# Performance work log

Hardware: AMD Instinct MI355X
Metric: run time of the kernel (lower is better)

Reference implementation:

```python
import jax, jax.numpy as jnp
import numpy as np

NUM_GRAPHS = 8
EV_A3_TO_GPA = 160.21766208


def _energy(pos, bond_vec, src, dst, edge_graph, centers, W1, b1, W2, b2, W3, b3):
    # Surrogate GNN energy: edge displacement mixes pos and bond_vec so both get grads,
    # mirroring grad(total_energies, [pos, bond_vec]) in the original wrapper.
    disp = bond_vec + pos[dst] - pos[src]                      # [E,3]
    d = jnp.sqrt(jnp.sum(disp * disp, axis=-1) + 1e-12)        # [E]
    rbf = jnp.exp(-jnp.square(d[:, None] - centers[None, :]))  # [E,K]
    h = jax.nn.silu(rbf @ W1 + b1)                             # [E,H]
    h = jax.nn.silu(h @ W2 + b2)                               # [E,H]
    e_edge = (h @ W3 + b3)[:, 0]                               # [E]
    return jax.ops.segment_sum(e_edge, edge_graph, num_segments=NUM_GRAPHS)  # [B]


def setup_inputs() -> dict:
    key = jax.random.key(0)
    ks = jax.random.split(key, 8)
    N, E, K, H = 49152, 786432, 32, 64
    pos = jax.random.normal(ks[0], (N, 3), jnp.float32) * 3.0
    bond_vec = jax.random.normal(ks[1], (E, 3), jnp.float32)
    src = jax.random.randint(ks[2], (E,), 0, N, dtype=jnp.int32)
    dst = jax.random.randint(ks[3], (E,), 0, N, dtype=jnp.int32)
    edge_graph = jnp.repeat(jnp.arange(NUM_GRAPHS, dtype=jnp.int32), E // NUM_GRAPHS)
    volume = jax.random.uniform(ks[4], (N,), jnp.float32, 50.0, 150.0)
    centers = jnp.linspace(0.0, 5.0, K).astype(jnp.float32)
    W1 = jax.random.normal(ks[5], (K, H), jnp.float32) / np.float32(np.sqrt(K))
    b1 = jnp.zeros((H,), jnp.float32)
    W2 = jax.random.normal(ks[6], (H, H), jnp.float32) / np.float32(np.sqrt(H))
    b2 = jnp.zeros((H,), jnp.float32)
    W3 = jax.random.normal(ks[7], (H, 1), jnp.float32) / np.float32(np.sqrt(H))
    b3 = jnp.zeros((1,), jnp.float32)
    return {"pos": pos, "bond_vec": bond_vec, "src": src, "dst": dst,
            "edge_graph": edge_graph, "volume": volume, "centers": centers,
            "W1": W1, "b1": b1, "W2": W2, "b2": b2, "W3": W3, "b3": b3}


def reference(pos, bond_vec, src, dst, edge_graph, volume, centers, W1, b1, W2, b2, W3, b3):
    energies, vjp_fn = jax.vjp(
        lambda p, bv: _energy(p, bv, src, dst, edge_graph, centers, W1, b1, W2, b2, W3, b3),
        pos, bond_vec)
    # grad_outputs = ones_like(total_energies)
    gpos, gbv = vjp_fn(jnp.ones_like(energies))
    forces = -gpos                                             # [N,3]
    f_ij = -gbv                                                # [E,3]
    # Per-graph stress: bond_vec_g^T @ f_ij_g, vectorized as segment-summed outer products.
    outer = bond_vec[:, :, None] * f_ij[:, None, :]            # [E,3,3]
    S = jax.ops.segment_sum(outer, edge_graph, num_segments=NUM_GRAPHS)  # [B,3,3]
    nodes_per_graph = pos.shape[0] // NUM_GRAPHS
    vol0 = volume[jnp.arange(NUM_GRAPHS) * nodes_per_graph]    # volume at first node of each graph
    stresses = (-EV_A3_TO_GPA * S / vol0[:, None, None]).reshape(NUM_GRAPHS * 3, 3)
    hessian = jnp.zeros((1,), jnp.float32)                     # calc_hessian=False
    return energies, forces, stresses, hessian
```

## Files before the change

kernel.cpp:

```cpp
#include <hip/hip_runtime.h>
#include <math.h>

#define K_RBF 32
#define H_DIM 64
#define TBL 4096
#define D_MAX 16.0f
#define N_NODES 49152
#define N_EDGES 786432
#define N_GRAPHS 8
#define NODES_PER_GRAPH 6144
#define EV_A3_TO_GPA 160.21766208f
#define LOG2E 1.44269504088896f

#define OUT_FORCES 8
#define OUT_STRESS 147464
#define OUT_TAIL_N 81

#define CHUNK_NODES  192
#define CHUNK_FLOATS 576
#define N_CHUNKS     256
#define REC_CAP      7168

#define EDGE_BLOCKS   384
#define EDGE_THREADS  1024
#define EDGES_PER_GRAPH (N_EDGES / N_GRAPHS)
#define BLK_PER_GRAPH 48

#define OFF_TAB 0u
#define OFF_CNT 32768u
#define OFF_REC 33792u
#define WS_NEED (OFF_REC + (size_t)N_CHUNKS * REC_CAP * 16u)

__device__ __forceinline__ int chunk_of(int node) {
    return (int)((unsigned)((node >> 6) * 683) >> 11);
}

__global__ __launch_bounds__(256) void build_table(
    const float* __restrict__ centers,
    const float* __restrict__ W1, const float* __restrict__ b1,
    const float* __restrict__ W2, const float* __restrict__ b2,
    const float* __restrict__ W3, const float* __restrict__ b3,
    float2* __restrict__ tab, int* __restrict__ gcnt,
    float* __restrict__ out, int zero_out_tail)
{
    if (blockIdx.x == 0) {
        int t = threadIdx.x;
        gcnt[t] = 0;
        if (zero_out_tail) {
            if (t < N_GRAPHS) out[t] = 0.f;
            else if (t < OUT_TAIL_N) out[3 * N_NODES + t] = 0.f;
        }
    }

    __shared__ float W2s[H_DIM * 65];
    for (int idx = threadIdx.x; idx < H_DIM * H_DIM; idx += 256)
        W2s[(idx >> 6) * 65 + (idx & 63)] = W2[idx];
    __syncthreads();

    int lane = threadIdx.x & 63;
    int i    = blockIdx.x * 4 + (threadIdx.x >> 6);
    float d  = (float)i * (D_MAX / (float)TBL);

    float z1 = b1[lane], u = 0.f;
#pragma unroll
    for (int k = 0; k < K_RBF; ++k) {
        float tc = d - centers[k];
        float e  = exp2f(-tc * tc * LOG2E);
        float w  = W1[k * H_DIM + lane];
        z1 = fmaf(e, w, z1);
        u  = fmaf(-2.f * tc * e, w, u);
    }
    float s1  = 1.f / (1.f + exp2f(-z1 * LOG2E));
    float h1  = z1 * s1;
    float ds1 = s1 * fmaf(z1, 1.f - s1, 1.f);

    float z2 = b2[lane];
#pragma unroll
    for (int h = 0; h < H_DIM; ++h)
        z2 = fmaf(__shfl(h1, h, 64), W2s[h * 65 + lane], z2);

    float s2  = 1.f / (1.f + exp2f(-z2 * LOG2E));
    float w3  = W3[lane];
    float Fp  = z2 * s2 * w3;
    float dz2 = w3 * s2 * fmaf(z2, 1.f - s2, 1.f);

    float dh1 = 0.f;
#pragma unroll
    for (int j = 0; j < H_DIM; ++j)
        dh1 = fmaf(__shfl(dz2, j, 64), W2s[lane * 65 + j], dh1);

    float Gp = dh1 * ds1 * u;
#pragma unroll
    for (int m = 32; m > 0; m >>= 1) {
        Fp += __shfl_xor(Fp, m, 64);
        Gp += __shfl_xor(Gp, m, 64);
    }
    if (lane == 0) tab[i] = make_float2(Fp + b3[0], Gp);
}

__global__ __launch_bounds__(EDGE_THREADS) void edge_compute(
    const float* __restrict__ pos, const float* __restrict__ bond,
    const int* __restrict__ src, const int* __restrict__ dst,
    const float* __restrict__ volume, const float2* __restrict__ tab,
    float4* __restrict__ recs, int* __restrict__ gcnt,
    float* __restrict__ out)
{
    __shared__ int   cnt[N_CHUNKS];
    __shared__ int   basech[N_CHUNKS];
    __shared__ float red[16][10];

    const int t = threadIdx.x;
    if (t < N_CHUNKS) cnt[t] = 0;
    __syncthreads();

    const int g = blockIdx.x & 7;
    const int w = blockIdx.x >> 3;
    const int base_e = g * EDGES_PER_GRAPH + w * (EDGE_THREADS * 2);

    float vacc[10];
#pragma unroll
    for (int q = 0; q < 10; ++q) vacc[q] = 0.f;

    int   edi[2], esi[2], es0[2], es1[2];
    float egx[2], egy[2], egz[2];

#pragma unroll
    for (int i = 0; i < 2; ++i) {
        int e  = base_e + i * EDGE_THREADS + t;
        int si = src[e], di = dst[e];
        float bx = bond[3 * e + 0], by = bond[3 * e + 1], bz = bond[3 * e + 2];
        float dx = bx + pos[3 * di + 0] - pos[3 * si + 0];
        float dy = by + pos[3 * di + 1] - pos[3 * si + 1];
        float dz = bz + pos[3 * di + 2] - pos[3 * si + 2];
        float d  = sqrtf(fmaf(dx, dx, fmaf(dy, dy, fmaf(dz, dz, 1e-12f))));

        float tt  = fminf(d * ((float)TBL / D_MAX), (float)(TBL - 1));
        int   ix  = min((int)tt, TBL - 2);
        float fr  = tt - (float)ix;
        float2 ta = tab[ix], tb2 = tab[ix + 1];
        float F = fmaf(fr, tb2.x - ta.x, ta.x);
        float G = fmaf(fr, tb2.y - ta.y, ta.y);

        float scl = G / d;
        float gx = scl * dx, gy = scl * dy, gz = scl * dz;
        egx[i] = gx; egy[i] = gy; egz[i] = gz;
        edi[i] = di; esi[i] = si;
        es0[i] = atomicAdd(&cnt[chunk_of(di)], 1);
        es1[i] = atomicAdd(&cnt[chunk_of(si)], 1);

        vacc[0] += F;
        vacc[1] = fmaf(bx, gx, vacc[1]); vacc[2] = fmaf(bx, gy, vacc[2]);
        vacc[3] = fmaf(bx, gz, vacc[3]); vacc[4] = fmaf(by, gx, vacc[4]);
        vacc[5] = fmaf(by, gy, vacc[5]); vacc[6] = fmaf(by, gz, vacc[6]);
        vacc[7] = fmaf(bz, gx, vacc[7]); vacc[8] = fmaf(bz, gy, vacc[8]);
        vacc[9] = fmaf(bz, gz, vacc[9]);
    }
    __syncthreads();
    if (t < N_CHUNKS) basech[t] = atomicAdd(&gcnt[t], cnt[t]);
    __syncthreads();
#pragma unroll
    for (int i = 0; i < 2; ++i) {
        int c0 = chunk_of(edi[i]), c1 = chunk_of(esi[i]);
        int l0 = edi[i] - c0 * CHUNK_NODES;
        int l1 = esi[i] - c1 * CHUNK_NODES;
        int p0 = basech[c0] + es0[i];
        int p1 = basech[c1] + es1[i];
        if (p0 < REC_CAP)
            recs[(size_t)c0 * REC_CAP + p0] =
                make_float4(-egx[i], -egy[i], -egz[i], __int_as_float(l0));
        if (p1 < REC_CAP)
            recs[(size_t)c1 * REC_CAP + p1] =
                make_float4(egx[i], egy[i], egz[i], __int_as_float(l1));
    }

#pragma unroll
    for (int q = 0; q < 10; ++q) {
        float x = vacc[q];
#pragma unroll
        for (int m = 32; m > 0; m >>= 1) x += __shfl_xor(x, m, 64);
        vacc[q] = x;
    }
    int wave = t >> 6;
    if ((t & 63) == 0)
#pragma unroll
        for (int q = 0; q < 10; ++q) red[wave][q] = vacc[q];
    __syncthreads();
    if (t < 10) {
        float tot = 0.f;
#pragma unroll
        for (int k = 0; k < 16; ++k) tot += red[k][t];
        if (t == 0) atomicAdd(out + g, tot);
        else {
            float vol = volume[g * NODES_PER_GRAPH];
            atomicAdd(out + OUT_STRESS + g * 9 + (t - 1),
                      tot * (EV_A3_TO_GPA / vol));
        }
    }
}

__global__ __launch_bounds__(512) void scatter_direct(
    const float4* __restrict__ recs, const int* __restrict__ gcnt,
    float* __restrict__ out)
{
    __shared__ float acc[CHUNK_FLOATS];
    const int t = threadIdx.x;
    if (t < CHUNK_FLOATS) acc[t] = 0.f;
    if (t < CHUNK_FLOATS - 512) acc[512 + t] = 0.f;
    __syncthreads();

    const int c = blockIdx.x;
    int total = min(gcnt[c], REC_CAP);
    const float4* seg = recs + (size_t)c * REC_CAP;
    for (int r = t; r < total; r += 512) {
        float4 rec = seg[r];
        int li = 3 * __float_as_int(rec.w);
        atomicAdd(&acc[li + 0], rec.x);
        atomicAdd(&acc[li + 1], rec.y);
        atomicAdd(&acc[li + 2], rec.z);
    }
    __syncthreads();

    if (t < CHUNK_FLOATS / 4) {
        float4* dst4 = (float4*)(out + OUT_FORCES + c * CHUNK_FLOATS);
        dst4[t] = ((const float4*)acc)[t];
    }
}

__global__ __launch_bounds__(256) void edge_fallback(
    const float* __restrict__ pos, const float* __restrict__ bond,
    const int* __restrict__ src, const int* __restrict__ dst,
    const float* __restrict__ volume, const float2* __restrict__ tab,
    float* __restrict__ out)
{
    __shared__ float red[4][10];
    int lb = (blockIdx.x & 7) * (EDGES_PER_GRAPH / 256) + (blockIdx.x >> 3);
    int g  = blockIdx.x & 7;
    int e  = lb * 256 + threadIdx.x;

    int si = src[e], di = dst[e];
    float bx = bond[3 * e + 0], by = bond[3 * e + 1], bz = bond[3 * e + 2];
    float dx = bx + pos[3 * di + 0] - pos[3 * si + 0];
    float dy = by + pos[3 * di + 1] - pos[3 * si + 1];
    float dz = bz + pos[3 * di + 2] - pos[3 * si + 2];
    float d  = sqrtf(fmaf(dx, dx, fmaf(dy, dy, fmaf(dz, dz, 1e-12f))));

    float tt  = fminf(d * ((float)TBL / D_MAX), (float)(TBL - 1));
    int   ix  = min((int)tt, TBL - 2);
    float fr  = tt - (float)ix;
    float2 ta = tab[ix], tb2 = tab[ix + 1];
    float F = fmaf(fr, tb2.x - ta.x, ta.x);
    float G = fmaf(fr, tb2.y - ta.y, ta.y);
    float scl = G / d;
    float gx = scl * dx, gy = scl * dy, gz = scl * dz;

    float* forces = out + OUT_FORCES;
    atomicAdd(forces + 3 * di + 0, -gx);
    atomicAdd(forces + 3 * di + 1, -gy);
    atomicAdd(forces + 3 * di + 2, -gz);
    atomicAdd(forces + 3 * si + 0,  gx);
    atomicAdd(forces + 3 * si + 1,  gy);
    atomicAdd(forces + 3 * si + 2,  gz);

    float v[10] = { F,
                    bx * gx, bx * gy, bx * gz,
                    by * gx, by * gy, by * gz,
                    bz * gx, bz * gy, bz * gz };
#pragma unroll
    for (int q = 0; q < 10; ++q) {
        float x = v[q];
#pragma unroll
        for (int m = 32; m > 0; m >>= 1) x += __shfl_xor(x, m, 64);
        v[q] = x;
    }
    int wave = threadIdx.x >> 6;
    if ((threadIdx.x & 63) == 0)
#pragma unroll
        for (int q = 0; q < 10; ++q) red[wave][q] = v[q];
    __syncthreads();
    if (threadIdx.x < 10) {
        float tot = red[0][threadIdx.x] + red[1][threadIdx.x]
                  + red[2][threadIdx.x] + red[3][threadIdx.x];
        if (threadIdx.x == 0) atomicAdd(out + g, tot);
        else {
            float vol = volume[g * NODES_PER_GRAPH];
            atomicAdd(out + OUT_STRESS + g * 9 + (threadIdx.x - 1),
                      tot * (EV_A3_TO_GPA / vol));
        }
    }
}

extern "C" void kernel_launch(void* const* d_in, const int* in_sizes, int n_in,
                              void* d_out, int out_size, void* d_ws, size_t ws_size,
                              hipStream_t stream)
{
    const float* pos     = (const float*)d_in[0];
    const float* bond    = (const float*)d_in[1];
    const int*   src     = (const int*)d_in[2];
    const int*   dst     = (const int*)d_in[3];
    const float* volume  = (const float*)d_in[5];
    const float* centers = (const float*)d_in[6];
    const float* W1 = (const float*)d_in[7];
    const float* b1 = (const float*)d_in[8];
    const float* W2 = (const float*)d_in[9];
    const float* b2 = (const float*)d_in[10];
    const float* W3 = (const float*)d_in[11];
    const float* b3 = (const float*)d_in[12];
    float*  out  = (float*)d_out;
    char*   ws   = (char*)d_ws;
    float2* tab  = (float2*)(ws + OFF_TAB);
    int*    gcnt = (int*)(ws + OFF_CNT);
    float4* recs = (float4*)(ws + OFF_REC);

    if (ws_size >= WS_NEED) {
        build_table<<<TBL / 4, 256, 0, stream>>>(centers, W1, b1, W2, b2, W3, b3,
                                                 tab, gcnt, out, 1);
        edge_compute<<<EDGE_BLOCKS, EDGE_THREADS, 0, stream>>>(
            pos, bond, src, dst, volume, tab, recs, gcnt, out);
        scatter_direct<<<N_CHUNKS, 512, 0, stream>>>(recs, gcnt, out);
    } else {
        hipMemsetAsync(d_out, 0, (size_t)out_size * sizeof(float), stream);
        build_table<<<TBL / 4, 256, 0, stream>>>(centers, W1, b1, W2, b2, W3, b3,
                                                 tab, gcnt, out, 0);
        edge_fallback<<<N_EDGES / 256, 256, 0, stream>>>(
            pos, bond, src, dst, volume, tab, out);
    }
}
```

Baseline: 150.7 us.

## Replace chunked record binning with per-node slots and gather reduction

Drops the chunked binning, where each block counted edges per 192-node chunk in shared memory and then claimed space with per-chunk global atomics, in favour of fixed per-node slots of capacity 96. Each edge endpoint now takes its slot with a global atomicAdd on a per-node counter. A new gather kernel uses four threads per node to sum that node's records and writes the forces directly, with no shared-memory float atomics. The trade is two returning global atomics per edge at random addresses, scattered record writes, and a much larger workspace. If the workspace is too small the slow fallback path runs, and records past 96 for a node are silently dropped.

```diff
diff --git a/kernel.cpp b/kernel.cpp
--- a/kernel.cpp
+++ b/kernel.cpp
@@ -16,10 +16,7 @@
 #define OUT_STRESS 147464
 #define OUT_TAIL_N 81
 
-#define CHUNK_NODES  192
-#define CHUNK_FLOATS 576
-#define N_CHUNKS     256
-#define REC_CAP      7168
+#define CAP_DEG 96
 
 #define EDGE_BLOCKS   384
 #define EDGE_THREADS  1024
@@ -28,37 +25,33 @@
 
 #define OFF_TAB 0u
 #define OFF_CNT 32768u
-#define OFF_REC 33792u
-#define WS_NEED (OFF_REC + (size_t)N_CHUNKS * REC_CAP * 16u)
-
-__device__ __forceinline__ int chunk_of(int node) {
-    return (int)((unsigned)((node >> 6) * 683) >> 11);
-}
+#define OFF_REC 229376u
+#define WS_NEED (OFF_REC + (size_t)N_NODES * CAP_DEG * 16u)
 
 __global__ __launch_bounds__(256) void build_table(
     const float* __restrict__ centers,
     const float* __restrict__ W1, const float* __restrict__ b1,
     const float* __restrict__ W2, const float* __restrict__ b2,
     const float* __restrict__ W3, const float* __restrict__ b3,
-    float2* __restrict__ tab, int* __restrict__ gcnt,
-    float* __restrict__ out, int zero_out_tail)
-{
-    if (blockIdx.x == 0) {
-        int t = threadIdx.x;
-        gcnt[t] = 0;
-        if (zero_out_tail) {
+    float2* __restrict__ tab, int* __restrict__ ncnt,
+    float* __restrict__ out, int main_path)
+{
+    const int t = threadIdx.x;
+    if (main_path) {
+        if (t < 48) ncnt[blockIdx.x * 48 + t] = 0;
+        if (blockIdx.x == 0) {
             if (t < N_GRAPHS) out[t] = 0.f;
             else if (t < OUT_TAIL_N) out[3 * N_NODES + t] = 0.f;
         }
     }
 
     __shared__ float W2s[H_DIM * 65];
-    for (int idx = threadIdx.x; idx < H_DIM * H_DIM; idx += 256)
+    for (int idx = t; idx < H_DIM * H_DIM; idx += 256)
         W2s[(idx >> 6) * 65 + (idx & 63)] = W2[idx];
     __syncthreads();
 
-    int lane = threadIdx.x & 63;
-    int i    = blockIdx.x * 4 + (threadIdx.x >> 6);
+    int lane = t & 63;
+    int i    = blockIdx.x * 4 + (t >> 6);
     float d  = (float)i * (D_MAX / (float)TBL);
 
     float z1 = b1[lane], u = 0.f;
@@ -102,17 +95,12 @@
     const float* __restrict__ pos, const float* __restrict__ bond,
     const int* __restrict__ src, const int* __restrict__ dst,
     const float* __restrict__ volume, const float2* __restrict__ tab,
-    float4* __restrict__ recs, int* __restrict__ gcnt,
+    float4* __restrict__ recs, int* __restrict__ ncnt,
     float* __restrict__ out)
 {
-    __shared__ int   cnt[N_CHUNKS];
-    __shared__ int   basech[N_CHUNKS];
     __shared__ float red[16][10];
 
     const int t = threadIdx.x;
-    if (t < N_CHUNKS) cnt[t] = 0;
-    __syncthreads();
-
     const int g = blockIdx.x & 7;
     const int w = blockIdx.x >> 3;
     const int base_e = g * EDGES_PER_GRAPH + w * (EDGE_THREADS * 2);
@@ -121,7 +109,7 @@
 #pragma unroll
     for (int q = 0; q < 10; ++q) vacc[q] = 0.f;
 
-    int   edi[2], esi[2], es0[2], es1[2];
+    int   edi[2], esi[2], ep0[2], ep1[2];
     float egx[2], egy[2], egz[2];
 
 #pragma unroll
@@ -145,8 +133,8 @@
         float gx = scl * dx, gy = scl * dy, gz = scl * dz;
         egx[i] = gx; egy[i] = gy; egz[i] = gz;
         edi[i] = di; esi[i] = si;
-        es0[i] = atomicAdd(&cnt[chunk_of(di)], 1);
-        es1[i] = atomicAdd(&cnt[chunk_of(si)], 1);
+        ep0[i] = atomicAdd(&ncnt[di], 1);
+        ep1[i] = atomicAdd(&ncnt[si], 1);
 
         vacc[0] += F;
         vacc[1] = fmaf(bx, gx, vacc[1]); vacc[2] = fmaf(bx, gy, vacc[2]);
@@ -155,22 +143,15 @@
         vacc[7] = fmaf(bz, gx, vacc[7]); vacc[8] = fmaf(bz, gy, vacc[8]);
         vacc[9] = fmaf(bz, gz, vacc[9]);
     }
-    __syncthreads();
-    if (t < N_CHUNKS) basech[t] = atomicAdd(&gcnt[t], cnt[t]);
-    __syncthreads();
+
 #pragma unroll
     for (int i = 0; i < 2; ++i) {
-        int c0 = chunk_of(edi[i]), c1 = chunk_of(esi[i]);
-        int l0 = edi[i] - c0 * CHUNK_NODES;
-        int l1 = esi[i] - c1 * CHUNK_NODES;
-        int p0 = basech[c0] + es0[i];
-        int p1 = basech[c1] + es1[i];
-        if (p0 < REC_CAP)
-            recs[(size_t)c0 * REC_CAP + p0] =
-                make_float4(-egx[i], -egy[i], -egz[i], __int_as_float(l0));
-        if (p1 < REC_CAP)
-            recs[(size_t)c1 * REC_CAP + p1] =
-                make_float4(egx[i], egy[i], egz[i], __int_as_float(l1));
+        if (ep0[i] < CAP_DEG)
+            recs[(size_t)edi[i] * CAP_DEG + ep0[i]] =
+                make_float4(-egx[i], -egy[i], -egz[i], 0.f);
+        if (ep1[i] < CAP_DEG)
+            recs[(size_t)esi[i] * CAP_DEG + ep1[i]] =
+                make_float4(egx[i], egy[i], egz[i], 0.f);
     }
 
 #pragma unroll
@@ -198,31 +179,29 @@
     }
 }
 
-__global__ __launch_bounds__(512) void scatter_direct(
-    const float4* __restrict__ recs, const int* __restrict__ gcnt,
+__global__ __launch_bounds__(256) void gather_forces(
+    const float4* __restrict__ recs, const int* __restrict__ ncnt,
     float* __restrict__ out)
 {
-    __shared__ float acc[CHUNK_FLOATS];
-    const int t = threadIdx.x;
-    if (t < CHUNK_FLOATS) acc[t] = 0.f;
-    if (t < CHUNK_FLOATS - 512) acc[512 + t] = 0.f;
-    __syncthreads();
-
-    const int c = blockIdx.x;
-    int total = min(gcnt[c], REC_CAP);
-    const float4* seg = recs + (size_t)c * REC_CAP;
-    for (int r = t; r < total; r += 512) {
-        float4 rec = seg[r];
-        int li = 3 * __float_as_int(rec.w);
-        atomicAdd(&acc[li + 0], rec.x);
-        atomicAdd(&acc[li + 1], rec.y);
-        atomicAdd(&acc[li + 2], rec.z);
-    }
-    __syncthreads();
-
-    if (t < CHUNK_FLOATS / 4) {
-        float4* dst4 = (float4*)(out + OUT_FORCES + c * CHUNK_FLOATS);
-        dst4[t] = ((const float4*)acc)[t];
+    const int tid  = blockIdx.x * 256 + threadIdx.x;
+    const int node = tid >> 2;
+    const int sub  = tid & 3;
+    if (node >= N_NODES) return;
+
+    const int cnt = min(ncnt[node], CAP_DEG);
+    const float4* seg = recs + (size_t)node * CAP_DEG;
+
+    float sx = 0.f, sy = 0.f, sz = 0.f;
+    for (int k = sub; k < cnt; k += 4) {
+        float4 r = seg[k];
+        sx += r.x; sy += r.y; sz += r.z;
+    }
+    sx += __shfl_xor(sx, 1, 64); sy += __shfl_xor(sy, 1, 64); sz += __shfl_xor(sz, 1, 64);
+    sx += __shfl_xor(sx, 2, 64); sy += __shfl_xor(sy, 2, 64); sz += __shfl_xor(sz, 2, 64);
+
+    if (sub < 3) {
+        float v = (sub == 0) ? sx : ((sub == 1) ? sy : sz);
+        out[OUT_FORCES + node * 3 + sub] = v;
     }
 }
 
@@ -308,19 +287,19 @@
     float*  out  = (float*)d_out;
     char*   ws   = (char*)d_ws;
     float2* tab  = (float2*)(ws + OFF_TAB);
-    int*    gcnt = (int*)(ws + OFF_CNT);
+    int*    ncnt = (int*)(ws + OFF_CNT);
     float4* recs = (float4*)(ws + OFF_REC);
 
     if (ws_size >= WS_NEED) {
         build_table<<<TBL / 4, 256, 0, stream>>>(centers, W1, b1, W2, b2, W3, b3,
-                                                 tab, gcnt, out, 1);
+                                                 tab, ncnt, out, 1);
         edge_compute<<<EDGE_BLOCKS, EDGE_THREADS, 0, stream>>>(
-            pos, bond, src, dst, volume, tab, recs, gcnt, out);
-        scatter_direct<<<N_CHUNKS, 512, 0, stream>>>(recs, gcnt, out);
+            pos, bond, src, dst, volume, tab, recs, ncnt, out);
+        gather_forces<<<(N_NODES * 4) / 256, 256, 0, stream>>>(recs, ncnt, out);
     } else {
         hipMemsetAsync(d_out, 0, (size_t)out_size * sizeof(float), stream);
         build_table<<<TBL / 4, 256, 0, stream>>>(centers, W1, b1, W2, b2, W3, b3,
-                                                 tab, gcnt, out, 0);
+                                                 tab, ncnt, out, 0);
         edge_fallback<<<N_EDGES / 256, 256, 0, stream>>>(
             pos, bond, src, dst, volume, tab, out);
     }
```

After: 200.0 us. +32.8%, slower.

## Replace LDS float atomics in force scatter with counting-sort segmented reduction

Applied to the files above, without the earlier changes.

The per-chunk force scatter now counts records per node using integer LDS atomics, prefix-scans the counts, places records into a sorted LDS buffer, and has one thread per (node, component) sum its contiguous segment. This replaces three float atomicAdds per record with one integer atomic plus a serial per-thread sum, and gives a deterministic summation order. The edge kernel also changes from 384x1024 to 512x768 blocks. The sort uses about 112 KB of LDS per block, which limits occupancy, and the final sum loops are unbalanced across threads when node degrees differ.

```diff
diff --git a/kernel.cpp b/kernel.cpp
--- a/kernel.cpp
+++ b/kernel.cpp
@@ -17,14 +17,16 @@
 #define OUT_TAIL_N 81
 
 #define CHUNK_NODES  192
-#define CHUNK_FLOATS 576
 #define N_CHUNKS     256
 #define REC_CAP      7168
 
-#define EDGE_BLOCKS   384
-#define EDGE_THREADS  1024
+#define EDGE_BLOCKS   512
+#define EDGE_THREADS  768
 #define EDGES_PER_GRAPH (N_EDGES / N_GRAPHS)
-#define BLK_PER_GRAPH 48
+#define BLK_PER_GRAPH 64
+
+#define SCT_THREADS 576
+#define SCT_ITERS   13
 
 #define OFF_TAB 0u
 #define OFF_CNT 32768u
@@ -107,7 +109,7 @@
 {
     __shared__ int   cnt[N_CHUNKS];
     __shared__ int   basech[N_CHUNKS];
-    __shared__ float red[16][10];
+    __shared__ float red[12][10];
 
     const int t = threadIdx.x;
     if (t < N_CHUNKS) cnt[t] = 0;
@@ -188,7 +190,7 @@
     if (t < 10) {
         float tot = 0.f;
 #pragma unroll
-        for (int k = 0; k < 16; ++k) tot += red[k][t];
+        for (int k = 0; k < 12; ++k) tot += red[k][t];
         if (t == 0) atomicAdd(out + g, tot);
         else {
             float vol = volume[g * NODES_PER_GRAPH];
@@ -198,31 +200,68 @@
     }
 }
 
-__global__ __launch_bounds__(512) void scatter_direct(
+__global__ __launch_bounds__(SCT_THREADS) void scatter_sort(
     const float4* __restrict__ recs, const int* __restrict__ gcnt,
     float* __restrict__ out)
 {
-    __shared__ float acc[CHUNK_FLOATS];
+    __shared__ float4 sorted[REC_CAP];
+    __shared__ int    cnt[CHUNK_NODES];
+    __shared__ int    scan[CHUNK_NODES];
+
     const int t = threadIdx.x;
-    if (t < CHUNK_FLOATS) acc[t] = 0.f;
-    if (t < CHUNK_FLOATS - 512) acc[512 + t] = 0.f;
-    __syncthreads();
-
     const int c = blockIdx.x;
-    int total = min(gcnt[c], REC_CAP);
+    if (t < CHUNK_NODES) cnt[t] = 0;
+    __syncthreads();
+
+    const int total = min(gcnt[c], REC_CAP);
     const float4* seg = recs + (size_t)c * REC_CAP;
-    for (int r = t; r < total; r += 512) {
-        float4 rec = seg[r];
-        int li = 3 * __float_as_int(rec.w);
-        atomicAdd(&acc[li + 0], rec.x);
-        atomicAdd(&acc[li + 1], rec.y);
-        atomicAdd(&acc[li + 2], rec.z);
-    }
-    __syncthreads();
-
-    if (t < CHUNK_FLOATS / 4) {
-        float4* dst4 = (float4*)(out + OUT_FORCES + c * CHUNK_FLOATS);
-        dst4[t] = ((const float4*)acc)[t];
+
+    float4 rv[SCT_ITERS];
+    int    rs[SCT_ITERS];
+    int    rl[SCT_ITERS];
+#pragma unroll
+    for (int it = 0; it < SCT_ITERS; ++it) {
+        int r = t + it * SCT_THREADS;
+        rl[it] = -1;
+        if (r < total) {
+            float4 rec = seg[r];
+            int li = __float_as_int(rec.w);
+            rv[it] = rec;
+            rl[it] = li;
+            rs[it] = atomicAdd(&cnt[li], 1);
+        }
+    }
+    __syncthreads();
+
+    if (t < CHUNK_NODES) scan[t] = cnt[t];
+    __syncthreads();
+    for (int off = 1; off < CHUNK_NODES; off <<= 1) {
+        int v = 0;
+        if (t < CHUNK_NODES) { v = scan[t]; if (t >= off) v += scan[t - off]; }
+        __syncthreads();
+        if (t < CHUNK_NODES) scan[t] = v;
+        __syncthreads();
+    }
+
+#pragma unroll
+    for (int it = 0; it < SCT_ITERS; ++it) {
+        if (rl[it] >= 0) {
+            int pos = scan[rl[it]] - cnt[rl[it]] + rs[it];
+            sorted[pos] = rv[it];
+        }
+    }
+    __syncthreads();
+
+    {
+        int n  = t / 3, cc = t - n * 3;
+        int b  = scan[n] - cnt[n];
+        int k  = cnt[n];
+        float s = 0.f;
+        for (int i = 0; i < k; ++i) {
+            float4 v = sorted[b + i];
+            s += (cc == 0) ? v.x : ((cc == 1) ? v.y : v.z);
+        }
+        out[OUT_FORCES + (c * CHUNK_NODES + n) * 3 + cc] = s;
     }
 }
 
@@ -316,7 +355,7 @@
                                                  tab, gcnt, out, 1);
         edge_compute<<<EDGE_BLOCKS, EDGE_THREADS, 0, stream>>>(
             pos, bond, src, dst, volume, tab, recs, gcnt, out);
-        scatter_direct<<<N_CHUNKS, 512, 0, stream>>>(recs, gcnt, out);
+        scatter_sort<<<N_CHUNKS, SCT_THREADS, 0, stream>>>(recs, gcnt, out);
     } else {
         hipMemsetAsync(d_out, 0, (size_t)out_size * sizeof(float), stream);
         build_table<<<TBL / 4, 256, 0, stream>>>(centers, W1, b1, W2, b2, W3, b3,
```

Result: slower. 154.1 us (+2.3%).

## Stage edge records in shared memory sorted by chunk before global write

Applied to the files above, without the earlier changes.

Each edge block now prefix-scans its per-chunk counts and places its gradient records into a chunk-sorted shared-memory staging buffer. It then writes them to global memory in order, so consecutive threads store to contiguous addresses within each chunk's record region instead of scattering. Block shape changes from 384x1024 to 512x768 threads so each block's staging buffer fits in LDS. The cost is extra shared memory (about 48 KB of float4 staging), a log-step scan with many barriers, and packing the chunk id into the record's w field.

```diff
diff --git a/kernel.cpp b/kernel.cpp
--- a/kernel.cpp
+++ b/kernel.cpp
@@ -21,10 +21,10 @@
 #define N_CHUNKS     256
 #define REC_CAP      7168
 
-#define EDGE_BLOCKS   384
-#define EDGE_THREADS  1024
+#define EDGE_BLOCKS   512
+#define EDGE_THREADS  768
 #define EDGES_PER_GRAPH (N_EDGES / N_GRAPHS)
-#define BLK_PER_GRAPH 48
+#define RECS_PER_BLOCK (EDGE_THREADS * 4)
 
 #define OFF_TAB 0u
 #define OFF_CNT 32768u
@@ -105,9 +105,11 @@
     float4* __restrict__ recs, int* __restrict__ gcnt,
     float* __restrict__ out)
 {
-    __shared__ int   cnt[N_CHUNKS];
-    __shared__ int   basech[N_CHUNKS];
-    __shared__ float red[16][10];
+    __shared__ float4 stage[RECS_PER_BLOCK];
+    __shared__ int    cnt[N_CHUNKS];
+    __shared__ int    incl[N_CHUNKS];
+    __shared__ int    basech[N_CHUNKS];
+    __shared__ float  red[12][10];
 
     const int t = threadIdx.x;
     if (t < N_CHUNKS) cnt[t] = 0;
@@ -156,21 +158,42 @@
         vacc[9] = fmaf(bz, gz, vacc[9]);
     }
     __syncthreads();
+
+    if (t < N_CHUNKS) incl[t] = cnt[t];
+    __syncthreads();
+#pragma unroll
+    for (int off = 1; off < N_CHUNKS; off <<= 1) {
+        int v = 0;
+        if (t < N_CHUNKS) { v = incl[t]; if (t >= off) v += incl[t - off]; }
+        __syncthreads();
+        if (t < N_CHUNKS) incl[t] = v;
+        __syncthreads();
+    }
     if (t < N_CHUNKS) basech[t] = atomicAdd(&gcnt[t], cnt[t]);
     __syncthreads();
+
 #pragma unroll
     for (int i = 0; i < 2; ++i) {
         int c0 = chunk_of(edi[i]), c1 = chunk_of(esi[i]);
         int l0 = edi[i] - c0 * CHUNK_NODES;
         int l1 = esi[i] - c1 * CHUNK_NODES;
-        int p0 = basech[c0] + es0[i];
-        int p1 = basech[c1] + es1[i];
-        if (p0 < REC_CAP)
-            recs[(size_t)c0 * REC_CAP + p0] =
-                make_float4(-egx[i], -egy[i], -egz[i], __int_as_float(l0));
-        if (p1 < REC_CAP)
-            recs[(size_t)c1 * REC_CAP + p1] =
-                make_float4(egx[i], egy[i], egz[i], __int_as_float(l1));
+        stage[incl[c0] - cnt[c0] + es0[i]] =
+            make_float4(-egx[i], -egy[i], -egz[i], __int_as_float((c0 << 8) | l0));
+        stage[incl[c1] - cnt[c1] + es1[i]] =
+            make_float4(egx[i], egy[i], egz[i], __int_as_float((c1 << 8) | l1));
+    }
+    __syncthreads();
+
+#pragma unroll
+    for (int it = 0; it < 4; ++it) {
+        int j = t + it * EDGE_THREADS;
+        float4 r = stage[j];
+        int wv = __float_as_int(r.w);
+        int c  = wv >> 8;
+        int p  = basech[c] + (j - (incl[c] - cnt[c]));
+        if (p < REC_CAP)
+            recs[(size_t)c * REC_CAP + p] =
+                make_float4(r.x, r.y, r.z, __int_as_float(wv & 255));
     }
 
 #pragma unroll
@@ -188,7 +211,7 @@
     if (t < 10) {
         float tot = 0.f;
 #pragma unroll
-        for (int k = 0; k < 16; ++k) tot += red[k][t];
+        for (int k = 0; k < 12; ++k) tot += red[k][t];
         if (t == 0) atomicAdd(out + g, tot);
         else {
             float vol = volume[g * NODES_PER_GRAPH];
```

Result: no change. 150.9 us (median of 2 runs) (+0.2%).
